# Kernel optimization log

Measured on AMD Instinct MI355X. Metric: run time of the kernel, lower is better.

## Reference

```python
import jax, jax.numpy as jnp
import numpy as np

N_NODES = 100000
N_EDGES = 1600000
D_FEAT = 128
HIDDEN = 128
HEADS = 4
OUT_C = HIDDEN // HEADS  # 32
N_CLASSES = 10
N_GRAPHS = 64
NEG_SLOPE = 0.2


def glorot(key, shape, fan_in, fan_out):
    s = jnp.sqrt(6.0 / (fan_in + fan_out))
    return jax.random.uniform(key, shape, minval=-s, maxval=s, dtype=jnp.float32)


def setup_inputs() -> dict:
    key = jax.random.key(0)
    ks = jax.random.split(key, 24)
    x = jax.random.normal(ks[0], (N_NODES, D_FEAT), dtype=jnp.float32)
    src = jax.random.randint(ks[1], (N_EDGES,), 0, N_NODES, dtype=jnp.int32)
    off = jax.random.randint(ks[2], (N_EDGES,), 1, N_NODES, dtype=jnp.int32)
    dst = ((src + off) % N_NODES).astype(jnp.int32)  # guarantees no self-loops
    edge_index = jnp.stack([src, dst], axis=0)
    batch = jnp.sort(jax.random.randint(ks[3], (N_NODES,), 0, N_GRAPHS, dtype=jnp.int32))
    inp = {"x": x, "edge_index": edge_index, "batch": batch}
    # GATConv layer params: W [in, H*C] (lin_l == lin_r), att_l/att_r [H, C], bias [H*C]
    ins = [D_FEAT, HIDDEN, HIDDEN]
    for i in range(3):
        k = 4 + 4 * i
        inp[f"W{i+1}"] = glorot(ks[k], (ins[i], HEADS * OUT_C), ins[i], HEADS * OUT_C)
        inp[f"al{i+1}"] = glorot(ks[k + 1], (HEADS, OUT_C), HEADS * OUT_C, 1)
        inp[f"ar{i+1}"] = glorot(ks[k + 2], (HEADS, OUT_C), HEADS * OUT_C, 1)
        inp[f"b{i+1}"] = jnp.zeros((HEADS * OUT_C,), jnp.float32)
    inp["lin1_w"] = glorot(ks[16], (HIDDEN, HIDDEN), HIDDEN, HIDDEN)
    inp["lin1_b"] = jnp.zeros((HIDDEN,), jnp.float32)
    inp["lin2_w"] = glorot(ks[17], (HIDDEN, N_CLASSES), HIDDEN, N_CLASSES)
    inp["lin2_b"] = jnp.zeros((N_CLASSES,), jnp.float32)
    return inp


def gat_layer(x, src, dst, W, att_l, att_r, bias):
    n = x.shape[0]
    H, C = att_l.shape
    xw = (x @ W).reshape(n, H, C)                       # Theta x
    al = jnp.einsum('nhc,hc->nh', xw, att_l)
    ar = jnp.einsum('nhc,hc->nh', xw, att_r)
    loop = jnp.arange(n, dtype=src.dtype)
    s = jnp.concatenate([src, loop])                    # add self-loops
    d = jnp.concatenate([dst, loop])
    logits = jax.nn.leaky_relu(al[s] + ar[d], NEG_SLOPE)  # [E+N, H]
    m = jax.ops.segment_max(logits, d, num_segments=n)    # segment softmax over dst
    e = jnp.exp(logits - m[d])
    z = jax.ops.segment_sum(e, d, num_segments=n)
    alpha = e / z[d]
    msg = xw[s] * alpha[:, :, None]                     # [E+N, H, C]
    out = jax.ops.segment_sum(msg, d, num_segments=n)   # scatter-add aggregate
    return out.reshape(n, H * C) + bias


def reference(x, edge_index, batch,
              W1, al1, ar1, b1, W2, al2, ar2, b2, W3, al3, ar3, b3,
              lin1_w, lin1_b, lin2_w, lin2_b):
    src, dst = edge_index[0], edge_index[1]
    h = jax.nn.relu(gat_layer(x, src, dst, W1, al1, ar1, b1))
    h = jax.nn.relu(gat_layer(h, src, dst, W2, al2, ar2, b2))
    h = jax.nn.relu(gat_layer(h, src, dst, W3, al3, ar3, b3))
    last = h
    # global mean pool over graphs in the batch
    s = jax.ops.segment_sum(h, batch, num_segments=N_GRAPHS)
    cnt = jax.ops.segment_sum(jnp.ones((h.shape[0],), h.dtype), batch, num_segments=N_GRAPHS)
    pooled = s / jnp.maximum(cnt, 1.0)[:, None]
    g = jax.nn.relu(pooled @ lin1_w + lin1_b)           # dropout inactive (eval)
    logits = g @ lin2_w + lin2_b
    return (jax.nn.log_softmax(logits, axis=-1), last)
```

## Files before the change

kernel.cpp:

```cpp
#include <hip/hip_runtime.h>
#include <math.h>


#define LRELU(x) ((x) > 0.f ? (x) : 0.2f*(x))
#define SH 8
#define TILE 4096
#define EPT 16

typedef __attribute__((ext_vector_type(8))) short s16x8;
typedef __attribute__((ext_vector_type(4))) float f32x4;

__device__ inline unsigned short f2bf(float f){
  unsigned u = __float_as_uint(f);
  u += 0x7fff + ((u >> 16) & 1);
  return (unsigned short)(u >> 16);
}

__global__ void k_init(int* __restrict__ bcnt, float* __restrict__ psum){
  int t = threadIdx.x;
  bcnt[t] = 0; bcnt[256 + t] = 0;
  for (int i = t; i < 8192; i += 256) psum[i] = 0.f;
}

template<bool BF16IN>
__device__ __forceinline__ void gemm_body(
    unsigned short* Wt, unsigned short* Xl,
    const void* __restrict__ Xv, const float* __restrict__ W,
    const float* __restrict__ attl, const float* __restrict__ attr,
    unsigned short* __restrict__ XW, float* __restrict__ AL, float* __restrict__ AR,
    int n, int bid, int gstride)
{
  int t = threadIdx.x;
  int lane = t & 63, w = t >> 6;
  int l15 = lane & 15, quad = lane >> 4;
  for (int i = 0; i < 64; i++){
    int e = i*256 + t;
    int k = e >> 7, nn = e & 127;
    Wt[nn*128 + ((((k>>3) ^ (nn&15))<<3) | (k&7))] = f2bf(W[e]);
  }
  int ntiles = (n + 63) >> 6;
  int r_ = t >> 2, seg = t & 3;
  for (int tile = bid; tile < ntiles; tile += gstride){
    int row0 = tile << 6;
    __syncthreads();
    {
      int grow = row0 + r_;
      unsigned short* dp = &Xl[r_*136 + seg*32];
      if (grow < n){
        if (BF16IN){
          const uint4* gp = (const uint4*)((const unsigned short*)Xv + (size_t)grow*128 + seg*32);
          #pragma unroll
          for (int i = 0; i < 4; i++) ((uint4*)dp)[i] = gp[i];
        } else {
          const float4* gp = (const float4*)((const float*)Xv + (size_t)grow*128 + seg*32);
          #pragma unroll
          for (int i = 0; i < 8; i++){
            float4 v = gp[i];
            ((unsigned*)dp)[i*2]   = (unsigned)f2bf(v.x) | ((unsigned)f2bf(v.y) << 16);
            ((unsigned*)dp)[i*2+1] = (unsigned)f2bf(v.z) | ((unsigned)f2bf(v.w) << 16);
          }
        }
      } else {
        #pragma unroll
        for (int i = 0; i < 4; i++) ((uint4*)dp)[i] = make_uint4(0,0,0,0);
      }
    }
    __syncthreads();
    f32x4 acc[4][2];
    #pragma unroll
    for (int rt = 0; rt < 4; rt++){ acc[rt][0] = (f32x4){0,0,0,0}; acc[rt][1] = (f32x4){0,0,0,0}; }
    #pragma unroll
    for (int ks = 0; ks < 4; ks++){
      s16x8 b0 = *(const s16x8*)&Wt[(w*32 + l15)*128      + (((ks*4+quad) ^ l15)<<3)];
      s16x8 b1 = *(const s16x8*)&Wt[(w*32 + 16 + l15)*128 + (((ks*4+quad) ^ l15)<<3)];
      #pragma unroll
      for (int rt = 0; rt < 4; rt++){
        s16x8 a = *(const s16x8*)&Xl[(rt*16 + l15)*136 + ks*32 + quad*8];
        acc[rt][0] = __builtin_amdgcn_mfma_f32_16x16x32_bf16(a, b0, acc[rt][0], 0, 0, 0);
        acc[rt][1] = __builtin_amdgcn_mfma_f32_16x16x32_bf16(a, b1, acc[rt][1], 0, 0, 0);
      }
    }
    __syncthreads();
    #pragma unroll
    for (int rt = 0; rt < 4; rt++)
      #pragma unroll
      for (int c2 = 0; c2 < 2; c2++)
        #pragma unroll
        for (int r = 0; r < 4; r++)
          Xl[(rt*16 + quad*4 + r)*136 + w*32 + c2*16 + l15] = f2bf(acc[rt][c2][r]);
    __syncthreads();
    {
      int grow = row0 + r_;
      if (grow < n){
        const unsigned short* sp = &Xl[r_*136 + seg*32];
        uint4 uu[4];
        #pragma unroll
        for (int i = 0; i < 4; i++) uu[i] = ((const uint4*)sp)[i];
        unsigned short* gx = XW + (size_t)grow*128 + seg*32;
        #pragma unroll
        for (int i = 0; i < 4; i++) ((uint4*)gx)[i] = uu[i];
        const unsigned* up = (const unsigned*)uu;
        const float4* alp = (const float4*)(attl + seg*32);
        const float4* arp = (const float4*)(attr + seg*32);
        float pl = 0.f, pr = 0.f;
        #pragma unroll
        for (int i = 0; i < 8; i++){
          unsigned ua = up[i*2], ub = up[i*2+1];
          float x0 = __uint_as_float(ua << 16);
          float x1 = __uint_as_float(ua & 0xffff0000u);
          float x2 = __uint_as_float(ub << 16);
          float x3 = __uint_as_float(ub & 0xffff0000u);
          float4 av = alp[i];
          float4 rv = arp[i];
          pl += x0*av.x + x1*av.y + x2*av.z + x3*av.w;
          pr += x0*rv.x + x1*rv.y + x2*rv.z + x3*rv.w;
        }
        AL[grow*4 + seg] = pl;
        AR[grow*4 + seg] = pr;
      }
    }
  }
}

template<bool BF16IN>
__global__ __launch_bounds__(256) void k_gemm(
    const void* __restrict__ Xv, const float* __restrict__ W,
    const float* __restrict__ attl, const float* __restrict__ attr,
    unsigned short* __restrict__ XW, float* __restrict__ AL, float* __restrict__ AR, int n)
{
  __shared__ unsigned short Wt[128*128];
  __shared__ unsigned short Xl[64*136];
  gemm_body<BF16IN>(Wt, Xl, Xv, W, attl, attr, XW, AL, AR, n, blockIdx.x, gridDim.x);
}

__global__ __launch_bounds__(256) void k_fuse1(
    const int* __restrict__ dst, int* __restrict__ bcnt, int E, int nparts,
    const float* __restrict__ X, const float* __restrict__ W,
    const float* __restrict__ attl, const float* __restrict__ attr,
    unsigned short* __restrict__ XW, float* __restrict__ AL, float* __restrict__ AR, int n)
{
  __shared__ unsigned short Wt[128*128];
  __shared__ unsigned short Xl[64*136];
  if ((int)blockIdx.x < nparts){
    int* lh = (int*)Wt;
    int t = threadIdx.x;
    for (int j = t; j < 512; j += 256) lh[j] = 0;
    __syncthreads();
    int base = blockIdx.x * TILE;
    int lim = min(base + TILE, E);
    for (int e = base + t; e < lim; e += 256)
      atomicAdd(&lh[dst[e] >> SH], 1);
    __syncthreads();
    for (int j = t; j < 512; j += 256){
      int v = lh[j];
      if (v) atomicAdd(&bcnt[j], v);
    }
    return;
  }
  gemm_body<false>(Wt, Xl, X, W, attl, attr, XW, AL, AR, n,
                   (int)blockIdx.x - nparts, (int)gridDim.x - nparts);
}

__global__ __launch_bounds__(256) void k_bscan(const int* __restrict__ bcnt,
    int* __restrict__ bstart, int* __restrict__ bfill, int NB, int E,
    const int* __restrict__ batch, int* __restrict__ gstart, int n){
  int t = threadIdx.x;
  if (blockIdx.x == 1){
    int g = t;
    if (g > 64) return;
    int lo = 0, hi = n;
    while (lo < hi){
      int mid = (lo + hi) >> 1;
      if (batch[mid] < g) lo = mid + 1; else hi = mid;
    }
    gstart[g] = lo;
    return;
  }
  __shared__ int c[512];
  __shared__ int ps[256];
  for (int j = t; j < 512; j += 256) c[j] = (j < NB) ? bcnt[j] : 0;
  __syncthreads();
  int b0 = 2*t;
  int v0 = c[b0], v1 = c[b0+1];
  int ts = v0 + v1;
  ps[t] = ts; __syncthreads();
  for (int off = 1; off < 256; off <<= 1){
    int x = (t >= off) ? ps[t-off] : 0; __syncthreads();
    ps[t] += x; __syncthreads();
  }
  int pre = ps[t] - ts;
  if (b0   < NB){ bstart[b0]   = pre;    bfill[b0]   = pre; }
  if (b0+1 < NB){ bstart[b0+1] = pre+v0; bfill[b0+1] = pre+v0; }
  if (t == 0) bstart[NB] = E;
}

__global__ __launch_bounds__(256) void k_part(const int* __restrict__ src,
    const int* __restrict__ dst, int* __restrict__ bfill,
    int2* __restrict__ tmp, int E){
  __shared__ int2 reorder[TILE];
  __shared__ int lhist[512], lscan[512], lgbase[512];
  __shared__ int ps[256];
  int t = threadIdx.x;
  int tb = blockIdx.x * TILE;
  int tilecnt = min(TILE, E - tb);
  for (int j = t; j < 512; j += 256) lhist[j] = 0;
  __syncthreads();
  int ss[EPT], dd[EPT], rk[EPT];
  #pragma unroll
  for (int i = 0; i < EPT; i++){
    int e = tb + t + i*256;
    if (e < E){
      ss[i] = src[e]; dd[i] = dst[e];
      rk[i] = atomicAdd(&lhist[dd[i] >> SH], 1);
    }
  }
  __syncthreads();
  int b0 = 2*t;
  int v0 = lhist[b0], v1 = lhist[b0+1];
  int ts = v0 + v1;
  ps[t] = ts; __syncthreads();
  for (int off = 1; off < 256; off <<= 1){
    int x = (t >= off) ? ps[t-off] : 0; __syncthreads();
    ps[t] += x; __syncthreads();
  }
  int pre = ps[t] - ts;
  int ex0 = pre, ex1 = pre + v0;
  lscan[b0] = ex0; lscan[b0+1] = ex1;
  if (v0 > 0){ int gb = atomicAdd(&bfill[b0],   v0); lgbase[b0]   = gb - ex0; }
  if (v1 > 0){ int gb = atomicAdd(&bfill[b0+1], v1); lgbase[b0+1] = gb - ex1; }
  __syncthreads();
  #pragma unroll
  for (int i = 0; i < EPT; i++){
    int e = tb + t + i*256;
    if (e < E){
      int b = dd[i] >> SH;
      reorder[lscan[b] + rk[i]] = make_int2(ss[i], dd[i]);
    }
  }
  __syncthreads();
  for (int j = t; j < tilecnt; j += 256){
    int2 p = reorder[j];
    tmp[lgbase[p.y >> SH] + j] = p;
  }
}

__global__ __launch_bounds__(256) void k_csr(const int2* __restrict__ tmp,
    const int* __restrict__ bstart, int* __restrict__ rp, int* __restrict__ col,
    int n, int E){
  __shared__ int lcnt[256];
  __shared__ int sc[256];
  int b = blockIdx.x, t = threadIdx.x;
  int node0 = b << SH;
  int ncnt = min(256, n - node0);
  int be = bstart[b], ee = bstart[b+1];
  lcnt[t] = 0;
  __syncthreads();
  for (int e = be + t; e < ee; e += 256)
    atomicAdd(&lcnt[tmp[e].y - node0], 1);
  __syncthreads();
  int v = lcnt[t];
  sc[t] = v;
  __syncthreads();
  for (int off = 1; off < 256; off <<= 1){
    int x = (t >= off) ? sc[t-off] : 0;
    __syncthreads();
    sc[t] += x;
    __syncthreads();
  }
  int start = be + sc[t] - v;
  lcnt[t] = start;
  if (t < ncnt) rp[node0 + t] = start;
  if (t == 0 && node0 + ncnt == n) rp[n] = E;
  __syncthreads();
  for (int e = be + t; e < ee; e += 256){
    int2 p = tmp[e];
    int pos = atomicAdd(&lcnt[p.y - node0], 1);
    col[pos] = p.x;
  }
}

template<bool BF16OUT>
__global__ __launch_bounds__(256) void k_attn(
    const unsigned short* __restrict__ XW, const float* __restrict__ AL, const float* __restrict__ AR,
    const int* __restrict__ rp, const int* __restrict__ col,
    const float* __restrict__ bias, void* __restrict__ OUT, int n)
{
  __shared__ float ebuf[4][64*4];
  __shared__ int   sbuf[4][64];
  int wv = threadIdx.x >> 6;
  int d = blockIdx.x*4 + wv;
  int lane = threadIdx.x & 63;
  if (d >= n) return;
  int start = rp[d], end = rp[d+1];
  float4 ald4 = ((const float4*)AL)[d];
  float4 ard4 = ((const float4*)AR)[d];
  float ar0 = ard4.x, ar1 = ard4.y, ar2 = ard4.z, ar3 = ard4.w;
  float es0 = __expf(LRELU(ald4.x + ar0));
  float es1 = __expf(LRELU(ald4.y + ar1));
  float es2 = __expf(LRELU(ald4.z + ar2));
  float es3 = __expf(LRELU(ald4.w + ar3));
  int h = lane >> 4;
  float eself = h==0?es0 : h==1?es1 : h==2?es2 : es3;
  const unsigned* XWr = (const unsigned*)XW;
  unsigned v = XWr[(unsigned)d*64 + lane];
  float acc0 = eself * __uint_as_float(v << 16);
  float acc1 = eself * __uint_as_float(v & 0xffff0000u);
  float zl0 = 0.f, zl1 = 0.f, zl2 = 0.f, zl3 = 0.f;
  float* eb = ebuf[wv];
  int*   sb = sbuf[wv];
  for (int base = start; base < end; base += 64){
    int cnt = min(64, end - base);
    int s = (lane < cnt) ? col[base + lane] : 0;
    float4 a = ((const float4*)AL)[s];
    float w0 = __expf(LRELU(a.x + ar0));
    float w1 = __expf(LRELU(a.y + ar1));
    float w2 = __expf(LRELU(a.z + ar2));
    float w3 = __expf(LRELU(a.w + ar3));
    if (lane >= cnt){ w0 = w1 = w2 = w3 = 0.f; }
    zl0 += w0; zl1 += w1; zl2 += w2; zl3 += w3;
    float4 w4; w4.x = w0; w4.y = w1; w4.z = w2; w4.w = w3;
    ((float4*)eb)[lane] = w4;
    sb[lane] = s << 6;
    #pragma unroll 8
    for (int j = 0; j < cnt; j++){
      unsigned sj = (unsigned)sb[j] + lane;
      float w = eb[j*4 + h];
      unsigned u = XWr[sj];
      acc0 = fmaf(w, __uint_as_float(u << 16), acc0);
      acc1 = fmaf(w, __uint_as_float(u & 0xffff0000u), acc1);
    }
  }
  #pragma unroll
  for (int off = 32; off >= 1; off >>= 1){
    zl0 += __shfl_xor(zl0, off, 64);
    zl1 += __shfl_xor(zl1, off, 64);
    zl2 += __shfl_xor(zl2, off, 64);
    zl3 += __shfl_xor(zl3, off, 64);
  }
  float z_h = (h==0?zl0 : h==1?zl1 : h==2?zl2 : zl3) + eself;
  float rz = 1.f / z_h;
  int ch = lane*2;
  float o0 = fmaf(acc0, rz, bias[ch]);
  float o1 = fmaf(acc1, rz, bias[ch+1]);
  o0 = o0 > 0.f ? o0 : 0.f;
  o1 = o1 > 0.f ? o1 : 0.f;
  if (BF16OUT){
    unsigned pk = (unsigned)f2bf(o0) | ((unsigned)f2bf(o1) << 16);
    ((unsigned*)OUT)[(unsigned)d*64 + lane] = pk;
  } else {
    float2 o; o.x = o0; o.y = o1;
    ((float2*)OUT)[(unsigned)d*64 + lane] = o;
  }
}

__global__ __launch_bounds__(128) void k_pool(const float* __restrict__ H,
                                              const int* __restrict__ gstart,
                                              float* __restrict__ psum){
  int g = blockIdx.x >> 3, slice = blockIdx.x & 7, t = threadIdx.x;
  int s0 = gstart[g], s1 = gstart[g+1];
  int cntg = s1 - s0;
  int chunk = (cntg + 7) >> 3;
  int lo = s0 + slice*chunk;
  int hi = min(lo + chunk, s1);
  float sum = 0.f;
  for (int i = lo; i < hi; i++) sum += H[(size_t)i*128 + t];
  atomicAdd(&psum[g*128 + t], sum);
}

__global__ __launch_bounds__(128) void k_mlp(const float* __restrict__ psum,
                       const int* __restrict__ gstart,
                       const float* __restrict__ w1, const float* __restrict__ b1,
                       const float* __restrict__ w2, const float* __restrict__ b2,
                       float* __restrict__ out)
{
  __shared__ float p[128];
  __shared__ float gsh[128];
  __shared__ float lg[10];
  int g = blockIdx.x, t = threadIdx.x;
  float c = fmaxf((float)(gstart[g+1] - gstart[g]), 1.f);
  p[t] = psum[g*128 + t] / c;
  __syncthreads();
  float acc = b1[t];
  for (int k = 0; k < 128; k++) acc = fmaf(p[k], w1[k*128 + t], acc);
  gsh[t] = acc > 0.f ? acc : 0.f;
  __syncthreads();
  if (t < 10){
    float a = b2[t];
    for (int k = 0; k < 128; k++) a = fmaf(gsh[k], w2[k*10 + t], a);
    lg[t] = a;
  }
  __syncthreads();
  if (t < 10){
    float mx = lg[0];
    for (int c2 = 1; c2 < 10; c2++) mx = fmaxf(mx, lg[c2]);
    float se = 0.f;
    for (int c2 = 0; c2 < 10; c2++) se += __expf(lg[c2] - mx);
    out[g*10 + t] = lg[t] - mx - logf(se);
  }
}

extern "C" void kernel_launch(void* const* d_in, const int* in_sizes, int n_in,
                              void* d_out, int out_size, void* d_ws, size_t ws_size,
                              hipStream_t stream)
{
  const float* x    = (const float*)d_in[0];
  const int* eidx   = (const int*)d_in[1];
  const int* batch  = (const int*)d_in[2];
  const float* W[3]  = {(const float*)d_in[3], (const float*)d_in[7],  (const float*)d_in[11]};
  const float* al[3] = {(const float*)d_in[4], (const float*)d_in[8],  (const float*)d_in[12]};
  const float* ar[3] = {(const float*)d_in[5], (const float*)d_in[9],  (const float*)d_in[13]};
  const float* bs[3] = {(const float*)d_in[6], (const float*)d_in[10], (const float*)d_in[14]};
  const float* l1w = (const float*)d_in[15];
  const float* l1b = (const float*)d_in[16];
  const float* l2w = (const float*)d_in[17];
  const float* l2b = (const float*)d_in[18];
  int E = in_sizes[1] / 2;
  int n = in_sizes[2];
  const int* srcp = eidx;
  const int* dstp = eidx + E;
  int NB = (n + 255) >> SH;

  char* wsp = (char*)d_ws;
  auto alloc = [&](size_t bytes){ void* p = (void*)wsp; wsp += (bytes + 255) & ~(size_t)255; return p; };
  unsigned short* xw   = (unsigned short*)alloc((size_t)n*128*2);
  unsigned short* hbuf = (unsigned short*)alloc((size_t)n*128*2);
  float* ALb  = (float*)alloc((size_t)n*4*4);
  float* ARb  = (float*)alloc((size_t)n*4*4);
  int* rp     = (int*)alloc((size_t)(n+1)*4);
  int* col    = (int*)alloc((size_t)E*4);
  int2* tmp   = (int2*)alloc((size_t)E*8);
  int* bcnt   = (int*)alloc(512*4);
  int* bstart = (int*)alloc(513*4);
  int* bfill  = (int*)alloc(512*4);
  float* psum = (float*)alloc(64*128*4);
  int* gstart = (int*)alloc(65*4);

  float* outlog = (float*)d_out;
  float* h3     = (float*)d_out + 64*10;

  int nparts = (E + TILE - 1) / TILE;

  k_init<<<1, 256, 0, stream>>>(bcnt, psum);
  k_fuse1<<<nparts + 768, 256, 0, stream>>>(dstp, bcnt, E, nparts,
                                            x, W[0], al[0], ar[0], xw, ALb, ARb, n);
  k_bscan<<<2, 256, 0, stream>>>(bcnt, bstart, bfill, NB, E, batch, gstart, n);
  k_part <<<nparts, 256, 0, stream>>>(srcp, dstp, bfill, tmp, E);
  k_csr  <<<NB, 256, 0, stream>>>(tmp, bstart, rp, col, n, E);

  k_attn<true><<<(n+3)/4, 256, 0, stream>>>(xw, ALb, ARb, rp, col, bs[0], hbuf, n);
  k_gemm<true><<<768, 256, 0, stream>>>(hbuf, W[1], al[1], ar[1], xw, ALb, ARb, n);
  k_attn<true><<<(n+3)/4, 256, 0, stream>>>(xw, ALb, ARb, rp, col, bs[1], hbuf, n);
  k_gemm<true><<<768, 256, 0, stream>>>(hbuf, W[2], al[2], ar[2], xw, ALb, ARb, n);
  k_attn<false><<<(n+3)/4, 256, 0, stream>>>(xw, ALb, ARb, rp, col, bs[2], h3, n);

  k_pool<<<64*8, 128, 0, stream>>>(h3, gstart, psum);
  k_mlp <<<64, 128, 0, stream>>>(psum, gstart, l1w, l1b, l2w, l2b, outlog);
}
```

Baseline: 580.9 us.

## Precompute bf16 weights, pack CSR temp, split attention lanes, fuse pooling into head

Several independent changes land together. Weight conversion to swizzled bf16 moves into the init kernel, so each GEMM block copies a ready tile instead of converting 16K floats. The CSR temp array is packed into 32-bit words (24-bit src plus 8-bit local dst) and staged in LDS in k_csr. The attention kernel has each half-wave handle alternate edges with 8-byte loads, combining the halves by shuffle. Pooling and the MLP are fused into one head kernel, the GEMM grid shrinks to 521 blocks, and the packing assumes node ids fit in 24 bits.

```diff
diff --git a/kernel.cpp b/kernel.cpp
--- a/kernel.cpp
+++ b/kernel.cpp
@@ -6,6 +6,7 @@
 #define SH 8
 #define TILE 4096
 #define EPT 16
+#define CSR_CAP 6144
 
 typedef __attribute__((ext_vector_type(8))) short s16x8;
 typedef __attribute__((ext_vector_type(4))) float f32x4;
@@ -16,16 +17,32 @@
   return (unsigned short)(u >> 16);
 }
 
-__global__ void k_init(int* __restrict__ bcnt, float* __restrict__ psum){
-  int t = threadIdx.x;
-  bcnt[t] = 0; bcnt[256 + t] = 0;
-  for (int i = t; i < 8192; i += 256) psum[i] = 0.f;
+__global__ __launch_bounds__(256) void k_init(int* __restrict__ bcnt,
+    const float* __restrict__ W1, const float* __restrict__ W2, const float* __restrict__ W3,
+    unsigned short* __restrict__ Wp){
+  int b = blockIdx.x, t = threadIdx.x;
+  if (b == 0){ bcnt[t] = 0; bcnt[256 + t] = 0; return; }
+  int l = (b - 1) >> 3, part = (b - 1) & 7;
+  const float* W = l == 0 ? W1 : l == 1 ? W2 : W3;
+  unsigned short* Wt = Wp + l*16384;
+  int id = part*256 + t;
+  int nn = id >> 4, c = id & 15;
+  unsigned u[4];
+  #pragma unroll
+  for (int qq = 0; qq < 4; qq++){
+    int k0 = 8*c + 2*qq;
+    unsigned short a = f2bf(W[(size_t)k0*128 + nn]);
+    unsigned short bb = f2bf(W[(size_t)(k0+1)*128 + nn]);
+    u[qq] = (unsigned)a | ((unsigned)bb << 16);
+  }
+  int off = nn*128 + ((c ^ (nn & 15)) << 3);
+  *((uint4*)(Wt + off)) = make_uint4(u[0], u[1], u[2], u[3]);
 }
 
 template<bool BF16IN>
 __device__ __forceinline__ void gemm_body(
     unsigned short* Wt, unsigned short* Xl,
-    const void* __restrict__ Xv, const float* __restrict__ W,
+    const void* __restrict__ Xv, const unsigned short* __restrict__ Wpre,
     const float* __restrict__ attl, const float* __restrict__ attr,
     unsigned short* __restrict__ XW, float* __restrict__ AL, float* __restrict__ AR,
     int n, int bid, int gstride)
@@ -33,11 +50,9 @@
   int t = threadIdx.x;
   int lane = t & 63, w = t >> 6;
   int l15 = lane & 15, quad = lane >> 4;
-  for (int i = 0; i < 64; i++){
-    int e = i*256 + t;
-    int k = e >> 7, nn = e & 127;
-    Wt[nn*128 + ((((k>>3) ^ (nn&15))<<3) | (k&7))] = f2bf(W[e]);
-  }
+  #pragma unroll
+  for (int i = 0; i < 8; i++)
+    ((uint4*)Wt)[i*256 + t] = ((const uint4*)Wpre)[i*256 + t];
   int ntiles = (n + 63) >> 6;
   int r_ = t >> 2, seg = t & 3;
   for (int tile = bid; tile < ntiles; tile += gstride){
@@ -124,18 +139,18 @@
 
 template<bool BF16IN>
 __global__ __launch_bounds__(256) void k_gemm(
-    const void* __restrict__ Xv, const float* __restrict__ W,
+    const void* __restrict__ Xv, const unsigned short* __restrict__ Wpre,
     const float* __restrict__ attl, const float* __restrict__ attr,
     unsigned short* __restrict__ XW, float* __restrict__ AL, float* __restrict__ AR, int n)
 {
   __shared__ unsigned short Wt[128*128];
   __shared__ unsigned short Xl[64*136];
-  gemm_body<BF16IN>(Wt, Xl, Xv, W, attl, attr, XW, AL, AR, n, blockIdx.x, gridDim.x);
+  gemm_body<BF16IN>(Wt, Xl, Xv, Wpre, attl, attr, XW, AL, AR, n, blockIdx.x, gridDim.x);
 }
 
 __global__ __launch_bounds__(256) void k_fuse1(
     const int* __restrict__ dst, int* __restrict__ bcnt, int E, int nparts,
-    const float* __restrict__ X, const float* __restrict__ W,
+    const float* __restrict__ X, const unsigned short* __restrict__ Wpre,
     const float* __restrict__ attl, const float* __restrict__ attr,
     unsigned short* __restrict__ XW, float* __restrict__ AL, float* __restrict__ AR, int n)
 {
@@ -157,7 +172,7 @@
     }
     return;
   }
-  gemm_body<false>(Wt, Xl, X, W, attl, attr, XW, AL, AR, n,
+  gemm_body<false>(Wt, Xl, X, Wpre, attl, attr, XW, AL, AR, n,
                    (int)blockIdx.x - nparts, (int)gridDim.x - nparts);
 }
 
@@ -196,7 +211,7 @@
 
 __global__ __launch_bounds__(256) void k_part(const int* __restrict__ src,
     const int* __restrict__ dst, int* __restrict__ bfill,
-    int2* __restrict__ tmp, int E){
+    unsigned* __restrict__ tmp, int E){
   __shared__ int2 reorder[TILE];
   __shared__ int lhist[512], lscan[512], lgbase[512];
   __shared__ int ps[256];
@@ -240,23 +255,28 @@
   __syncthreads();
   for (int j = t; j < tilecnt; j += 256){
     int2 p = reorder[j];
-    tmp[lgbase[p.y >> SH] + j] = p;
-  }
-}
-
-__global__ __launch_bounds__(256) void k_csr(const int2* __restrict__ tmp,
+    tmp[lgbase[p.y >> SH] + j] = (unsigned)p.x | ((unsigned)(p.y & 255) << 24);
+  }
+}
+
+__global__ __launch_bounds__(256) void k_csr(const unsigned* __restrict__ tmp,
     const int* __restrict__ bstart, int* __restrict__ rp, int* __restrict__ col,
     int n, int E){
+  __shared__ unsigned stage[CSR_CAP];
   __shared__ int lcnt[256];
   __shared__ int sc[256];
   int b = blockIdx.x, t = threadIdx.x;
   int node0 = b << SH;
   int ncnt = min(256, n - node0);
   int be = bstart[b], ee = bstart[b+1];
+  int cnt = ee - be;
   lcnt[t] = 0;
   __syncthreads();
-  for (int e = be + t; e < ee; e += 256)
-    atomicAdd(&lcnt[tmp[e].y - node0], 1);
+  for (int i = t; i < cnt; i += 256){
+    unsigned v = tmp[be + i];
+    if (i < CSR_CAP) stage[i] = v;
+    atomicAdd(&lcnt[v >> 24], 1);
+  }
   __syncthreads();
   int v = lcnt[t];
   sc[t] = v;
@@ -272,10 +292,10 @@
   if (t < ncnt) rp[node0 + t] = start;
   if (t == 0 && node0 + ncnt == n) rp[n] = E;
   __syncthreads();
-  for (int e = be + t; e < ee; e += 256){
-    int2 p = tmp[e];
-    int pos = atomicAdd(&lcnt[p.y - node0], 1);
-    col[pos] = p.x;
+  for (int i = t; i < cnt; i += 256){
+    unsigned u = (i < CSR_CAP) ? stage[i] : tmp[be + i];
+    int pos = atomicAdd(&lcnt[u >> 24], 1);
+    col[pos] = (int)(u & 0xFFFFFFu);
   }
 }
 
@@ -292,6 +312,8 @@
   int lane = threadIdx.x & 63;
   if (d >= n) return;
   int start = rp[d], end = rp[d+1];
+  int pair = lane >> 5, sub = lane & 31;
+  int h2 = sub >> 3;
   float4 ald4 = ((const float4*)AL)[d];
   float4 ard4 = ((const float4*)AR)[d];
   float ar0 = ard4.x, ar1 = ard4.y, ar2 = ard4.z, ar3 = ard4.w;
@@ -299,12 +321,16 @@
   float es1 = __expf(LRELU(ald4.y + ar1));
   float es2 = __expf(LRELU(ald4.z + ar2));
   float es3 = __expf(LRELU(ald4.w + ar3));
-  int h = lane >> 4;
-  float eself = h==0?es0 : h==1?es1 : h==2?es2 : es3;
-  const unsigned* XWr = (const unsigned*)XW;
-  unsigned v = XWr[(unsigned)d*64 + lane];
-  float acc0 = eself * __uint_as_float(v << 16);
-  float acc1 = eself * __uint_as_float(v & 0xffff0000u);
+  float eself = h2==0?es0 : h2==1?es1 : h2==2?es2 : es3;
+  const uint2* XW2 = (const uint2*)XW;
+  float acc0 = 0.f, acc1 = 0.f, acc2 = 0.f, acc3 = 0.f;
+  if (pair == 0){
+    uint2 xv = XW2[(unsigned)d*32 + sub];
+    acc0 = eself * __uint_as_float(xv.x << 16);
+    acc1 = eself * __uint_as_float(xv.x & 0xffff0000u);
+    acc2 = eself * __uint_as_float(xv.y << 16);
+    acc3 = eself * __uint_as_float(xv.y & 0xffff0000u);
+  }
   float zl0 = 0.f, zl1 = 0.f, zl2 = 0.f, zl3 = 0.f;
   float* eb = ebuf[wv];
   int*   sb = sbuf[wv];
@@ -320,14 +346,17 @@
     zl0 += w0; zl1 += w1; zl2 += w2; zl3 += w3;
     float4 w4; w4.x = w0; w4.y = w1; w4.z = w2; w4.w = w3;
     ((float4*)eb)[lane] = w4;
-    sb[lane] = s << 6;
-    #pragma unroll 8
-    for (int j = 0; j < cnt; j++){
-      unsigned sj = (unsigned)sb[j] + lane;
-      float w = eb[j*4 + h];
-      unsigned u = XWr[sj];
-      acc0 = fmaf(w, __uint_as_float(u << 16), acc0);
-      acc1 = fmaf(w, __uint_as_float(u & 0xffff0000u), acc1);
+    sb[lane] = s << 5;
+    #pragma unroll 4
+    for (int j = 0; j < cnt; j += 2){
+      int j0 = j + pair;
+      float w = eb[j0*4 + h2];
+      unsigned sj = (unsigned)sb[j0] + sub;
+      uint2 u = XW2[sj];
+      acc0 = fmaf(w, __uint_as_float(u.x << 16), acc0);
+      acc1 = fmaf(w, __uint_as_float(u.x & 0xffff0000u), acc1);
+      acc2 = fmaf(w, __uint_as_float(u.y << 16), acc2);
+      acc3 = fmaf(w, __uint_as_float(u.y & 0xffff0000u), acc3);
     }
   }
   #pragma unroll
@@ -337,52 +366,62 @@
     zl2 += __shfl_xor(zl2, off, 64);
     zl3 += __shfl_xor(zl3, off, 64);
   }
-  float z_h = (h==0?zl0 : h==1?zl1 : h==2?zl2 : zl3) + eself;
-  float rz = 1.f / z_h;
-  int ch = lane*2;
-  float o0 = fmaf(acc0, rz, bias[ch]);
-  float o1 = fmaf(acc1, rz, bias[ch+1]);
-  o0 = o0 > 0.f ? o0 : 0.f;
-  o1 = o1 > 0.f ? o1 : 0.f;
-  if (BF16OUT){
-    unsigned pk = (unsigned)f2bf(o0) | ((unsigned)f2bf(o1) << 16);
-    ((unsigned*)OUT)[(unsigned)d*64 + lane] = pk;
-  } else {
-    float2 o; o.x = o0; o.y = o1;
-    ((float2*)OUT)[(unsigned)d*64 + lane] = o;
-  }
-}
-
-__global__ __launch_bounds__(128) void k_pool(const float* __restrict__ H,
-                                              const int* __restrict__ gstart,
-                                              float* __restrict__ psum){
-  int g = blockIdx.x >> 3, slice = blockIdx.x & 7, t = threadIdx.x;
-  int s0 = gstart[g], s1 = gstart[g+1];
-  int cntg = s1 - s0;
-  int chunk = (cntg + 7) >> 3;
-  int lo = s0 + slice*chunk;
-  int hi = min(lo + chunk, s1);
-  float sum = 0.f;
-  for (int i = lo; i < hi; i++) sum += H[(size_t)i*128 + t];
-  atomicAdd(&psum[g*128 + t], sum);
-}
-
-__global__ __launch_bounds__(128) void k_mlp(const float* __restrict__ psum,
-                       const int* __restrict__ gstart,
-                       const float* __restrict__ w1, const float* __restrict__ b1,
-                       const float* __restrict__ w2, const float* __restrict__ b2,
-                       float* __restrict__ out)
-{
-  __shared__ float p[128];
+  acc0 += __shfl_xor(acc0, 32, 64);
+  acc1 += __shfl_xor(acc1, 32, 64);
+  acc2 += __shfl_xor(acc2, 32, 64);
+  acc3 += __shfl_xor(acc3, 32, 64);
+  if (pair == 0){
+    float z_h = (h2==0?zl0 : h2==1?zl1 : h2==2?zl2 : zl3) + eself;
+    float rz = 1.f / z_h;
+    float4 b4 = ((const float4*)bias)[sub];
+    float o0 = fmaf(acc0, rz, b4.x);
+    float o1 = fmaf(acc1, rz, b4.y);
+    float o2 = fmaf(acc2, rz, b4.z);
+    float o3 = fmaf(acc3, rz, b4.w);
+    o0 = o0 > 0.f ? o0 : 0.f;
+    o1 = o1 > 0.f ? o1 : 0.f;
+    o2 = o2 > 0.f ? o2 : 0.f;
+    o3 = o3 > 0.f ? o3 : 0.f;
+    if (BF16OUT){
+      uint2 pk;
+      pk.x = (unsigned)f2bf(o0) | ((unsigned)f2bf(o1) << 16);
+      pk.y = (unsigned)f2bf(o2) | ((unsigned)f2bf(o3) << 16);
+      ((uint2*)OUT)[(unsigned)d*32 + sub] = pk;
+    } else {
+      float4 o; o.x = o0; o.y = o1; o.z = o2; o.w = o3;
+      ((float4*)OUT)[(unsigned)d*32 + sub] = o;
+    }
+  }
+}
+
+__global__ __launch_bounds__(256) void k_head(const float* __restrict__ H,
+    const int* __restrict__ gstart,
+    const float* __restrict__ w1, const float* __restrict__ b1,
+    const float* __restrict__ w2, const float* __restrict__ b2,
+    float* __restrict__ out)
+{
+  __shared__ float p[256];
   __shared__ float gsh[128];
   __shared__ float lg[10];
   int g = blockIdx.x, t = threadIdx.x;
-  float c = fmaxf((float)(gstart[g+1] - gstart[g]), 1.f);
-  p[t] = psum[g*128 + t] / c;
-  __syncthreads();
-  float acc = b1[t];
-  for (int k = 0; k < 128; k++) acc = fmaf(p[k], w1[k*128 + t], acc);
-  gsh[t] = acc > 0.f ? acc : 0.f;
+  int c = t & 127, half = t >> 7;
+  int s0 = gstart[g], s1 = gstart[g+1];
+  float sum = 0.f;
+  for (int i = s0 + half; i < s1; i += 2)
+    sum += H[(size_t)i*128 + c];
+  p[t] = sum;
+  __syncthreads();
+  if (t < 128){
+    float cn = fmaxf((float)(s1 - s0), 1.f);
+    float pv = (p[t] + p[t + 128]) / cn;
+    p[t] = pv;
+  }
+  __syncthreads();
+  if (t < 128){
+    float acc = b1[t];
+    for (int k = 0; k < 128; k++) acc = fmaf(p[k], w1[k*128 + t], acc);
+    gsh[t] = acc > 0.f ? acc : 0.f;
+  }
   __syncthreads();
   if (t < 10){
     float a = b2[t];
@@ -428,31 +467,31 @@
   float* ARb  = (float*)alloc((size_t)n*4*4);
   int* rp     = (int*)alloc((size_t)(n+1)*4);
   int* col    = (int*)alloc((size_t)E*4);
-  int2* tmp   = (int2*)alloc((size_t)E*8);
+  unsigned* tmp = (unsigned*)alloc((size_t)E*4);
+  unsigned short* Wp = (unsigned short*)alloc(3*16384*2);
   int* bcnt   = (int*)alloc(512*4);
   int* bstart = (int*)alloc(513*4);
   int* bfill  = (int*)alloc(512*4);
-  float* psum = (float*)alloc(64*128*4);
   int* gstart = (int*)alloc(65*4);
 
   float* outlog = (float*)d_out;
   float* h3     = (float*)d_out + 64*10;
 
   int nparts = (E + TILE - 1) / TILE;
-
-  k_init<<<1, 256, 0, stream>>>(bcnt, psum);
-  k_fuse1<<<nparts + 768, 256, 0, stream>>>(dstp, bcnt, E, nparts,
-                                            x, W[0], al[0], ar[0], xw, ALb, ARb, n);
+  const int GG = 521;
+
+  k_init<<<25, 256, 0, stream>>>(bcnt, W[0], W[1], W[2], Wp);
+  k_fuse1<<<nparts + GG, 256, 0, stream>>>(dstp, bcnt, E, nparts,
+                                           x, Wp, al[0], ar[0], xw, ALb, ARb, n);
   k_bscan<<<2, 256, 0, stream>>>(bcnt, bstart, bfill, NB, E, batch, gstart, n);
   k_part <<<nparts, 256, 0, stream>>>(srcp, dstp, bfill, tmp, E);
   k_csr  <<<NB, 256, 0, stream>>>(tmp, bstart, rp, col, n, E);
 
   k_attn<true><<<(n+3)/4, 256, 0, stream>>>(xw, ALb, ARb, rp, col, bs[0], hbuf, n);
-  k_gemm<true><<<768, 256, 0, stream>>>(hbuf, W[1], al[1], ar[1], xw, ALb, ARb, n);
+  k_gemm<true><<<GG, 256, 0, stream>>>(hbuf, Wp + 16384, al[1], ar[1], xw, ALb, ARb, n);
   k_attn<true><<<(n+3)/4, 256, 0, stream>>>(xw, ALb, ARb, rp, col, bs[1], hbuf, n);
-  k_gemm<true><<<768, 256, 0, stream>>>(hbuf, W[2], al[2], ar[2], xw, ALb, ARb, n);
+  k_gemm<true><<<GG, 256, 0, stream>>>(hbuf, Wp + 32768, al[2], ar[2], xw, ALb, ARb, n);
   k_attn<false><<<(n+3)/4, 256, 0, stream>>>(xw, ALb, ARb, rp, col, bs[2], h3, n);
 
-  k_pool<<<64*8, 128, 0, stream>>>(h3, gstart, psum);
-  k_mlp <<<64, 128, 0, stream>>>(psum, gstart, l1w, l1b, l2w, l2b, outlog);
-}
+  k_head<<<64, 256, 0, stream>>>(h3, gstart, l1w, l1b, l2w, l2b, outlog);
+}
```

New measurement: 697.3 us. +20.1%, slower.
